# Kernel tuning notes

Measured on AMD Instinct MI355X. Metric: run time of the kernel, lower is better.

The kernel has to match this reference:

```python
import jax, jax.numpy as jnp
import numpy as np

N_HEAD = 16
D_MODEL = 1024
D_HEAD = 64
SCALE = 1.0 / D_HEAD ** 0.5
LN_EPS = 1e-5


def layer_norm(x, g, b):
    mu = jnp.mean(x, axis=-1, keepdims=True)
    var = jnp.mean(jnp.square(x - mu), axis=-1, keepdims=True)
    return (x - mu) * jax.lax.rsqrt(var + LN_EPS) * g + b


def setup_inputs() -> dict:
    key = jax.random.key(0)
    ks = jax.random.split(key, 6)
    T, B = 2048, 4
    h = jax.random.normal(ks[0], (T, B, D_MODEL), dtype=jnp.float32)
    # key-padding mask, shape (klen, bsz); True = masked
    attn_mask = jax.random.randint(ks[1], (T, B), 0, 2).astype(jnp.bool_)
    s = 1.0 / np.sqrt(D_MODEL)
    wq = jax.random.uniform(ks[2], (N_HEAD * D_HEAD, D_MODEL), minval=-s, maxval=s, dtype=jnp.float32)
    wkv = jax.random.uniform(ks[3], (2 * N_HEAD * D_HEAD, D_MODEL), minval=-s, maxval=s, dtype=jnp.float32)
    wo = jax.random.uniform(ks[4], (D_MODEL, N_HEAD * D_HEAD), minval=-s, maxval=s, dtype=jnp.float32)
    ln_g = jnp.ones((D_MODEL,), jnp.float32)
    ln_b = jnp.zeros((D_MODEL,), jnp.float32)
    return {"h": h, "attn_mask": attn_mask, "wq": wq, "wkv": wkv,
            "wo": wo, "ln_g": ln_g, "ln_b": ln_b}


def reference(h, attn_mask, wq, wkv, wo, ln_g, ln_b):
    T, B, _ = h.shape
    c = h  # mems is None
    head_q = (h @ wq.T).reshape(T, B, N_HEAD, D_HEAD)
    kv = c @ wkv.T
    head_k, head_v = jnp.split(kv, 2, axis=-1)
    head_k = head_k.reshape(T, B, N_HEAD, D_HEAD)
    head_v = head_v.reshape(T, B, N_HEAD, D_HEAD)

    # scores: [qlen, klen, bsz, n_head]
    attn_score = jnp.einsum('ibnd,jbnd->ijbn', head_q, head_k) * SCALE
    attn_score = jnp.where(attn_mask[None, :, :, None], -jnp.inf, attn_score)
    attn_prob = jax.nn.softmax(attn_score, axis=1)

    attn_vec = jnp.einsum('ijbn,jbnd->ibnd', attn_prob, head_v)
    attn_vec = attn_vec.reshape(T, B, N_HEAD * D_HEAD)
    attn_out = attn_vec @ wo.T
    # post-lnorm residual (pre_lnorm=False); gate='plus' path unused here
    return layer_norm(h + attn_out, ln_g, ln_b)
```

## Files before the change

### kernel.cpp

```cpp
#include <hip/hip_runtime.h>

#define T_LEN 2048
#define BSZ 4
#define NHEAD 16
#define DHEAD 64
#define DMODEL 1024
#define SCALE 0.125f
#define L2E_SCALE (0.125f * 1.44269504f)
#define ROW 72

typedef __bf16 bf16x8 __attribute__((ext_vector_type(8)));
typedef float f32x4 __attribute__((ext_vector_type(4)));

__device__ __forceinline__ float bf2f(unsigned short u) {
  union { unsigned int i; float f; } v; v.i = ((unsigned int)u) << 16; return v.f;
}
__device__ __forceinline__ unsigned short f2bf(float f) {
  union { float f; unsigned int i; } v; v.f = f;
  unsigned int r = v.i + 0x7fffu + ((v.i >> 16) & 1u);
  return (unsigned short)(r >> 16);
}

typedef __attribute__((address_space(1))) void* gptr_t;
typedef __attribute__((address_space(3))) void* lptr_t;

__device__ __forceinline__ void load_lds16(const void* g, void* l) {
  __builtin_amdgcn_global_load_lds((gptr_t)g, (lptr_t)l, 16, 0, 0);
}

__global__ __launch_bounds__(256) void cvt_prep(const float* __restrict__ h,
                                                const float* __restrict__ wq,
                                                const float* __restrict__ wkv,
                                                const float* __restrict__ wo,
                                                const unsigned char* __restrict__ mask,
                                                unsigned short* __restrict__ h_bf,
                                                unsigned short* __restrict__ wq_bf,
                                                unsigned short* __restrict__ wkv_bf,
                                                unsigned short* __restrict__ wo_bf,
                                                int* __restrict__ pos,
                                                int* __restrict__ nkeys) {
  const int tid = threadIdx.x;
  if (blockIdx.x < 12288) {
    const size_t E4 = (size_t)T_LEN * BSZ * DMODEL / 4;
    const size_t W4 = (size_t)NHEAD * DHEAD * DMODEL / 4;
    const size_t g = (size_t)blockIdx.x * 256 + tid;
    const float* src; unsigned short* dst; size_t off;
    if (g < E4)                { src = h;   dst = h_bf;   off = g; }
    else if (g < E4 + W4)      { src = wq;  dst = wq_bf;  off = g - E4; }
    else if (g < E4 + 3 * W4)  { src = wkv; dst = wkv_bf; off = g - E4 - W4; }
    else                       { src = wo;  dst = wo_bf;  off = g - E4 - 3 * W4; }
    const float4 v = *(const float4*)(src + off * 4);
    ushort4 o;
    o.x = f2bf(v.x); o.y = f2bf(v.y); o.z = f2bf(v.z); o.w = f2bf(v.w);
    *(ushort4*)(dst + off * 4) = o;
    return;
  }
  __shared__ int s_any;
  if (tid == 0) s_any = 0;
  __syncthreads();
  int acc = 0;
  for (int i = tid; i < T_LEN * BSZ; i += 256)
    if ((i & 3) != 0 && mask[i] != 0) acc = 1;
  if (acc) atomicOr(&s_any, 1);
  __syncthreads();
  const int mmode = s_any ? 0 : 1;
  const int wv = tid >> 6, lane = tid & 63;
  const int b = wv;
  int run = 0;
  for (int j0 = 0; j0 < T_LEN; j0 += 64) {
    const int j = j0 + lane;
    const int mval = mmode ? ((const int*)mask)[(size_t)j * BSZ + b]
                           : (int)mask[(size_t)j * BSZ + b];
    const int keep = (mval == 0) ? 1 : 0;
    int x = keep;
#pragma unroll
    for (int off = 1; off < 64; off <<= 1) {
      const int y = __shfl_up(x, off, 64);
      if (lane >= off) x += y;
    }
    pos[b * T_LEN + j] = keep ? (run + x - keep) : -1;
    run += __shfl(x, 63, 64);
  }
  if (lane == 0) nkeys[b] = run;
}

#define GEMM64_BODY(Aptr, Bptr)                                                        \
  const int tid  = threadIdx.x;                                                        \
  const int lane = tid & 63;                                                           \
  const int wv   = tid >> 6;                                                           \
  const int wr = (wv >> 1) * 64;                                                       \
  const int wc = (wv & 1) * 64;                                                        \
  const int mi   = lane & 15;                                                          \
  const int quad = lane >> 4;                                                          \
  f32x4 acc[4][4] = {};                                                                \
  int rowc[4], colc[4];                                                                \
  _Pragma("unroll")                                                                    \
  for (int c = 0; c < 4; c++) {                                                        \
    const int s = c * 256 + tid;                                                       \
    rowc[c] = s >> 3;                                                                  \
    colc[c] = ((s & 7) ^ (rowc[c] & 7)) * 8;                                           \
  }                                                                                    \
  const int swz = mi & 7;                                                              \
  for (int k0 = 0; k0 < DMODEL; k0 += 64) {                                            \
    _Pragma("unroll")                                                                  \
    for (int c = 0; c < 4; c++) {                                                      \
      load_lds16(Aptr + (size_t)rowc[c] * DMODEL + k0 + colc[c], As + c * 2048 + wv * 512); \
      load_lds16(Bptr + (size_t)rowc[c] * DMODEL + k0 + colc[c], Bs + c * 2048 + wv * 512); \
    }                                                                                  \
    __syncthreads();                                                                   \
    _Pragma("unroll")                                                                  \
    for (int kq = 0; kq < 2; kq++) {                                                   \
      const int cp = ((kq * 4 + quad) ^ swz) * 8;                                      \
      bf16x8 af[4], bfr[4];                                                            \
      _Pragma("unroll")                                                                \
      for (int rt = 0; rt < 4; rt++)                                                   \
        af[rt] = *(const bf16x8*)(As + (wr + rt * 16 + mi) * 64 + cp);                 \
      _Pragma("unroll")                                                                \
      for (int ct = 0; ct < 4; ct++)                                                   \
        bfr[ct] = *(const bf16x8*)(Bs + (wc + ct * 16 + mi) * 64 + cp);                \
      _Pragma("unroll")                                                                \
      for (int rt = 0; rt < 4; rt++)                                                   \
        _Pragma("unroll")                                                              \
        for (int ct = 0; ct < 4; ct++)                                                 \
          acc[rt][ct] = __builtin_amdgcn_mfma_f32_16x16x32_bf16(af[rt], bfr[ct], acc[rt][ct], 0, 0, 0); \
    }                                                                                  \
    __syncthreads();                                                                   \
  }

__global__ __launch_bounds__(256) void gemm_qkv(const unsigned short* __restrict__ A,
                                                const unsigned short* __restrict__ Wq,
                                                const unsigned short* __restrict__ Wkv,
                                                const int* __restrict__ pos,
                                                unsigned short* __restrict__ outQ,
                                                unsigned short* __restrict__ outK,
                                                unsigned short* __restrict__ outVt) {
  __shared__ alignas(16) unsigned short As[128 * 64];
  __shared__ alignas(16) unsigned short Bs[128 * 64];
  const int m0 = blockIdx.y * 128;
  const int n0 = blockIdx.x * 128;
  const unsigned short* Abase = A + (size_t)m0 * DMODEL;
  const unsigned short* Bbase = (n0 < DMODEL) ? (Wq + (size_t)n0 * DMODEL)
                                              : (Wkv + (size_t)(n0 - DMODEL) * DMODEL);
  GEMM64_BODY(Abase, Bbase)

  const int region = n0 >> 10;
#pragma unroll
  for (int rt = 0; rt < 4; rt++) {
#pragma unroll
    for (int r = 0; r < 4; r++) {
      const int gm = m0 + wr + rt * 16 + quad * 4 + r;
      const int i = gm >> 2, b = gm & 3;
      int p = i;
      if (region > 0) p = pos[b * T_LEN + i];
      if (region > 0 && p < 0) continue;
#pragma unroll
      for (int ct = 0; ct < 4; ct++) {
        const int gn = n0 + wc + ct * 16 + mi;
        const int gnl = gn & (DMODEL - 1);
        const int hn = gnl >> 6, d = gnl & 63;
        const float v = acc[rt][ct][r];
        if (region == 0)
          outQ[(((size_t)b * NHEAD + hn) * T_LEN + i) * DHEAD + d] = f2bf(v * L2E_SCALE);
        else if (region == 1)
          outK[(((size_t)b * NHEAD + hn) * T_LEN + p) * DHEAD + d] = f2bf(v);
        else
          outVt[(((size_t)b * NHEAD + hn) * DHEAD + d) * T_LEN + p] = f2bf(v);
      }
    }
  }
}

__global__ __launch_bounds__(256) void gemm_out(const unsigned short* __restrict__ A,
                                                const unsigned short* __restrict__ Bw,
                                                unsigned short* __restrict__ outB) {
  __shared__ alignas(16) unsigned short As[128 * 64];
  __shared__ alignas(16) unsigned short Bs[128 * 64];
  const int m0 = blockIdx.y * 128;
  const int n0 = blockIdx.x * 128;
  const unsigned short* Abase = A  + (size_t)m0 * DMODEL;
  const unsigned short* Bbase = Bw + (size_t)n0 * DMODEL;
  GEMM64_BODY(Abase, Bbase)

#pragma unroll
  for (int rt = 0; rt < 4; rt++)
#pragma unroll
    for (int ct = 0; ct < 4; ct++)
#pragma unroll
      for (int r = 0; r < 4; r++) {
        const int gm = m0 + wr + rt * 16 + quad * 4 + r;
        const int gn = n0 + wc + ct * 16 + mi;
        outB[(size_t)gm * DMODEL + gn] = f2bf(acc[rt][ct][r]);
      }
}

template<bool TAIL>
__device__ __forceinline__ void attn_chunk(int j0, int nk, int mi, int quad,
    const unsigned short* Ks, const unsigned short* Vts, unsigned short* PsW,
    const bf16x8 (&qb)[2][2], f32x4 (&oc)[2][4], float (&rs)[2]) {
  f32x4 sc[2][4] = {};
#pragma unroll
  for (int ct = 0; ct < 4; ct++) {
    const bf16x8 kf0 = *(const bf16x8*)(Ks + (ct * 16 + mi) * ROW + quad * 8);
    const bf16x8 kf1 = *(const bf16x8*)(Ks + (ct * 16 + mi) * ROW + 32 + quad * 8);
#pragma unroll
    for (int g = 0; g < 2; g++) {
      sc[g][ct] = __builtin_amdgcn_mfma_f32_16x16x32_bf16(kf0, qb[g][0], sc[g][ct], 0, 0, 0);
      sc[g][ct] = __builtin_amdgcn_mfma_f32_16x16x32_bf16(kf1, qb[g][1], sc[g][ct], 0, 0, 0);
    }
  }
#pragma unroll
  for (int g = 0; g < 2; g++)
#pragma unroll
    for (int ct = 0; ct < 4; ct++) {
#pragma unroll
      for (int r = 0; r < 4; r++) {
        float p = __builtin_amdgcn_exp2f(sc[g][ct][r]);
        if (TAIL && (j0 + ct * 16 + quad * 4 + r >= nk)) p = 0.f;
        rs[g] += p;
        sc[g][ct][r] = p;
      }
      union { float f; unsigned u; } c0, c1, c2, c3;
      c0.f = sc[g][ct][0]; c1.f = sc[g][ct][1]; c2.f = sc[g][ct][2]; c3.f = sc[g][ct][3];
      const unsigned pk0 = (c0.u >> 16) | (c1.u & 0xFFFF0000u);
      const unsigned pk1 = (c2.u >> 16) | (c3.u & 0xFFFF0000u);
      *(uint2*)(PsW + (g * 16 + mi) * ROW + ct * 16 + quad * 4) = make_uint2(pk0, pk1);
    }
  bf16x8 pa0[2], pa1[2];
#pragma unroll
  for (int g = 0; g < 2; g++) {
    pa0[g] = *(const bf16x8*)(PsW + (g * 16 + mi) * ROW + quad * 8);
    pa1[g] = *(const bf16x8*)(PsW + (g * 16 + mi) * ROW + 32 + quad * 8);
  }
#pragma unroll
  for (int ct = 0; ct < 4; ct++) {
    const bf16x8 vf0 = *(const bf16x8*)(Vts + (ct * 16 + mi) * ROW + quad * 8);
    const bf16x8 vf1 = *(const bf16x8*)(Vts + (ct * 16 + mi) * ROW + 32 + quad * 8);
#pragma unroll
    for (int g = 0; g < 2; g++) {
      oc[g][ct] = __builtin_amdgcn_mfma_f32_16x16x32_bf16(pa0[g], vf0, oc[g][ct], 0, 0, 0);
      oc[g][ct] = __builtin_amdgcn_mfma_f32_16x16x32_bf16(pa1[g], vf1, oc[g][ct], 0, 0, 0);
    }
  }
}

__global__ __launch_bounds__(256, 4) void attn_mfma(const unsigned short* __restrict__ Qg,
                                                    const unsigned short* __restrict__ Kg,
                                                    const unsigned short* __restrict__ Vtg,
                                                    const int* __restrict__ nkeys,
                                                    unsigned short* __restrict__ av) {
  __shared__ alignas(16) unsigned short smem[18688];
  unsigned short* Ks  = smem;
  unsigned short* Vts = smem + 4608;
  unsigned short* Qs  = smem + 9216;
  float* Ls = (float*)(smem + 18432);

  const int tid  = threadIdx.x;
  const int lane = tid & 63;
  const int wv   = tid >> 6;
  const int mi   = lane & 15;
  const int quad = lane >> 4;
  const int i0 = blockIdx.x * 128;
  const int b  = blockIdx.y;
  const int n  = blockIdx.z;
  const size_t base = ((size_t)b * NHEAD + n) * T_LEN * DHEAD;
  const int nk = nkeys[b];

  for (int it = tid; it < 1024; it += 256) {
    const int r = it >> 3, c8 = (it & 7) * 8;
    *(uint4*)(Qs + r * ROW + c8) = *(const uint4*)(Qg + base + (size_t)(i0 + r) * DHEAD + c8);
  }
  __syncthreads();
  bf16x8 qb[2][2];
#pragma unroll
  for (int g = 0; g < 2; g++) {
    qb[g][0] = *(const bf16x8*)(Qs + (wv * 32 + g * 16 + mi) * ROW + quad * 8);
    qb[g][1] = *(const bf16x8*)(Qs + (wv * 32 + g * 16 + mi) * ROW + 32 + quad * 8);
  }

  f32x4 oc[2][4] = {};
  float rs[2] = {0.f, 0.f};
  unsigned short* PsW = Qs + wv * 2304;

  const int nmain = nk & ~63;
  for (int j0 = 0; j0 < nmain; j0 += 64) {
    for (int it = tid; it < 512; it += 256) {
      const int r = it >> 3, c8 = (it & 7) * 8;
      *(uint4*)(Ks  + r * ROW + c8) = *(const uint4*)(Kg  + base + (size_t)(j0 + r) * DHEAD + c8);
      *(uint4*)(Vts + r * ROW + c8) = *(const uint4*)(Vtg + base + (size_t)r * T_LEN + j0 + c8);
    }
    __syncthreads();
    attn_chunk<false>(j0, nk, mi, quad, Ks, Vts, PsW, qb, oc, rs);
    __syncthreads();
  }
  if (nmain < nk) {
    for (int it = tid; it < 512; it += 256) {
      const int r = it >> 3, c8 = (it & 7) * 8;
      *(uint4*)(Ks  + r * ROW + c8) = *(const uint4*)(Kg  + base + (size_t)(nmain + r) * DHEAD + c8);
      *(uint4*)(Vts + r * ROW + c8) = *(const uint4*)(Vtg + base + (size_t)r * T_LEN + nmain + c8);
    }
    __syncthreads();
    attn_chunk<true>(nmain, nk, mi, quad, Ks, Vts, PsW, qb, oc, rs);
  }

#pragma unroll
  for (int g = 0; g < 2; g++) {
    float t = rs[g];
    t += __shfl_xor(t, 16, 64);
    t += __shfl_xor(t, 32, 64);
    rs[g] = t;
  }
  if (quad == 0) { Ls[wv * 32 + mi] = rs[0]; Ls[wv * 32 + 16 + mi] = rs[1]; }
  __syncthreads();
  float linv[2][4];
#pragma unroll
  for (int g = 0; g < 2; g++)
#pragma unroll
    for (int r = 0; r < 4; r++) {
      const float l = Ls[wv * 32 + g * 16 + quad * 4 + r];
      linv[g][r] = (l > 0.f) ? (1.f / l) : 0.f;
    }
#pragma unroll
  for (int g = 0; g < 2; g++)
#pragma unroll
    for (int ct = 0; ct < 4; ct++)
#pragma unroll
      for (int r = 0; r < 4; r++) {
        const int q = i0 + wv * 32 + g * 16 + quad * 4 + r;
        const int d = ct * 16 + mi;
        av[((size_t)q * BSZ + b) * DMODEL + n * DHEAD + d] = f2bf(oc[g][ct][r] * linv[g][r]);
      }
}

__global__ __launch_bounds__(256) void ln_kernel(const float* __restrict__ h,
                                                 const unsigned short* __restrict__ ao,
                                                 const float* __restrict__ g,
                                                 const float* __restrict__ bb,
                                                 float* __restrict__ out) {
  __shared__ float red[16];
  const int row = blockIdx.x;
  const int tid = threadIdx.x;
  const size_t base = (size_t)row * DMODEL;
  float x[4];
  float s = 0.f, sq = 0.f;
#pragma unroll
  for (int k = 0; k < 4; k++) {
    const int c = tid + k * 256;
    const float xv = h[base + c] + bf2f(ao[base + c]);
    x[k] = xv; s += xv; sq += xv * xv;
  }
#pragma unroll
  for (int off = 32; off; off >>= 1) { s += __shfl_xor(s, off, 64); sq += __shfl_xor(sq, off, 64); }
  const int wv = tid >> 6, lane = tid & 63;
  if (lane == 0) { red[wv] = s; red[8 + wv] = sq; }
  __syncthreads();
  if (tid == 0) {
    float ts = 0.f, tq = 0.f;
    for (int w = 0; w < 4; w++) { ts += red[w]; tq += red[8 + w]; }
    red[4] = ts; red[12] = tq;
  }
  __syncthreads();
  const float mu  = red[4] * (1.f / DMODEL);
  const float var = red[12] * (1.f / DMODEL) - mu * mu;
  const float inv = rsqrtf(var + 1e-5f);
#pragma unroll
  for (int k = 0; k < 4; k++) {
    const int c = tid + k * 256;
    out[base + c] = (x[k] - mu) * inv * g[c] + bb[c];
  }
}

extern "C" void kernel_launch(void* const* d_in, const int* in_sizes, int n_in,
                              void* d_out, int out_size, void* d_ws, size_t ws_size,
                              hipStream_t stream) {
  (void)in_sizes; (void)n_in; (void)out_size; (void)ws_size;
  const float* h           = (const float*)d_in[0];
  const unsigned char* msk = (const unsigned char*)d_in[1];
  const float* wq          = (const float*)d_in[2];
  const float* wkv         = (const float*)d_in[3];
  const float* wo          = (const float*)d_in[4];
  const float* lng         = (const float*)d_in[5];
  const float* lnb         = (const float*)d_in[6];
  float* out = (float*)d_out;

  const size_t E  = (size_t)T_LEN * BSZ * DMODEL;
  const size_t WQ = (size_t)NHEAD * DHEAD * DMODEL;
  char* ws = (char*)d_ws;
  int* nkeys            = (int*)ws;                       ws += 16;
  int* pos              = (int*)ws;                       ws += (size_t)BSZ * T_LEN * 4;
  unsigned short* h_bf  = (unsigned short*)ws;            ws += E * 2;
  unsigned short* wq_bf = (unsigned short*)ws;            ws += WQ * 2;
  unsigned short* wkv_bf= (unsigned short*)ws;            ws += 2 * WQ * 2;
  unsigned short* wo_bf = (unsigned short*)ws;            ws += WQ * 2;
  unsigned short* Qb    = (unsigned short*)ws;            ws += E * 2;
  unsigned short* Kb    = (unsigned short*)ws;            ws += E * 2;
  unsigned short* Vtb   = (unsigned short*)ws;            ws += E * 2;
  unsigned short* AV    = (unsigned short*)ws;            ws += E * 2;
  unsigned short* AO    = (unsigned short*)ws;

  const dim3 blk(256);
  cvt_prep<<<dim3(12289), blk, 0, stream>>>(h, wq, wkv, wo, msk,
                                            h_bf, wq_bf, wkv_bf, wo_bf, pos, nkeys);
  gemm_qkv<<<dim3(3 * DMODEL / 128, T_LEN * BSZ / 128), blk, 0, stream>>>(
      h_bf, wq_bf, wkv_bf, pos, Qb, Kb, Vtb);
  attn_mfma<<<dim3(T_LEN / 128, BSZ, NHEAD), blk, 0, stream>>>(Qb, Kb, Vtb, nkeys, AV);
  gemm_out<<<dim3(DMODEL / 128, T_LEN * BSZ / 128), blk, 0, stream>>>(AV, wo_bf, AO);
  ln_kernel<<<dim3(T_LEN * BSZ), blk, 0, stream>>>(h, AO, lng, lnb, out);
}
```

Baseline: 319.9 us.

## Double-buffer LDS tiles in GEMMs and vectorize layernorm loads/stores

The shared GEMM body now uses two LDS buffers, issuing global-to-LDS loads for the next K-tile before computing on the current one. This hides load latency and needs one barrier per iteration instead of two. The price is twice the LDS per block (64KB), which may lower occupancy. Separately, the layernorm kernel now uses float4 and ushort4 vector loads and stores instead of strided scalar accesses.

```diff
diff --git a/kernel.cpp b/kernel.cpp
--- a/kernel.cpp
+++ b/kernel.cpp
@@ -84,7 +84,7 @@
   if (lane == 0) nkeys[b] = run;
 }
 
-#define GEMM64_BODY(Aptr, Bptr)                                                        \
+#define GEMM64_DBUF(Aptr, Bptr)                                                        \
   const int tid  = threadIdx.x;                                                        \
   const int lane = tid & 63;                                                           \
   const int wv   = tid >> 6;                                                           \
@@ -101,30 +101,41 @@
     colc[c] = ((s & 7) ^ (rowc[c] & 7)) * 8;                                           \
   }                                                                                    \
   const int swz = mi & 7;                                                              \
+  _Pragma("unroll")                                                                    \
+  for (int c = 0; c < 4; c++) {                                                        \
+    load_lds16(Aptr + (size_t)rowc[c] * DMODEL + colc[c], As + c * 2048 + wv * 512);   \
+    load_lds16(Bptr + (size_t)rowc[c] * DMODEL + colc[c], Bs + c * 2048 + wv * 512);   \
+  }                                                                                    \
   for (int k0 = 0; k0 < DMODEL; k0 += 64) {                                            \
-    _Pragma("unroll")                                                                  \
-    for (int c = 0; c < 4; c++) {                                                      \
-      load_lds16(Aptr + (size_t)rowc[c] * DMODEL + k0 + colc[c], As + c * 2048 + wv * 512); \
-      load_lds16(Bptr + (size_t)rowc[c] * DMODEL + k0 + colc[c], Bs + c * 2048 + wv * 512); \
+    const int cur = (k0 >> 6) & 1;                                                     \
+    const unsigned short* Asr = As + cur * 8192;                                       \
+    const unsigned short* Bsr = Bs + cur * 8192;                                       \
+    unsigned short* Asw = As + (1 - cur) * 8192;                                       \
+    unsigned short* Bsw = Bs + (1 - cur) * 8192;                                       \
+    __syncthreads();                                                                   \
+    if (k0 + 64 < DMODEL) {                                                            \
+      _Pragma("unroll")                                                                \
+      for (int c = 0; c < 4; c++) {                                                    \
+        load_lds16(Aptr + (size_t)rowc[c] * DMODEL + k0 + 64 + colc[c], Asw + c * 2048 + wv * 512); \
+        load_lds16(Bptr + (size_t)rowc[c] * DMODEL + k0 + 64 + colc[c], Bsw + c * 2048 + wv * 512); \
+      }                                                                                \
     }                                                                                  \
-    __syncthreads();                                                                   \
     _Pragma("unroll")                                                                  \
     for (int kq = 0; kq < 2; kq++) {                                                   \
       const int cp = ((kq * 4 + quad) ^ swz) * 8;                                      \
       bf16x8 af[4], bfr[4];                                                            \
       _Pragma("unroll")                                                                \
       for (int rt = 0; rt < 4; rt++)                                                   \
-        af[rt] = *(const bf16x8*)(As + (wr + rt * 16 + mi) * 64 + cp);                 \
+        af[rt] = *(const bf16x8*)(Asr + (wr + rt * 16 + mi) * 64 + cp);                \
       _Pragma("unroll")                                                                \
       for (int ct = 0; ct < 4; ct++)                                                   \
-        bfr[ct] = *(const bf16x8*)(Bs + (wc + ct * 16 + mi) * 64 + cp);                \
+        bfr[ct] = *(const bf16x8*)(Bsr + (wc + ct * 16 + mi) * 64 + cp);               \
       _Pragma("unroll")                                                                \
       for (int rt = 0; rt < 4; rt++)                                                   \
         _Pragma("unroll")                                                              \
         for (int ct = 0; ct < 4; ct++)                                                 \
           acc[rt][ct] = __builtin_amdgcn_mfma_f32_16x16x32_bf16(af[rt], bfr[ct], acc[rt][ct], 0, 0, 0); \
     }                                                                                  \
-    __syncthreads();                                                                   \
   }
 
 __global__ __launch_bounds__(256) void gemm_qkv(const unsigned short* __restrict__ A,
@@ -134,14 +145,14 @@
                                                 unsigned short* __restrict__ outQ,
                                                 unsigned short* __restrict__ outK,
                                                 unsigned short* __restrict__ outVt) {
-  __shared__ alignas(16) unsigned short As[128 * 64];
-  __shared__ alignas(16) unsigned short Bs[128 * 64];
+  __shared__ alignas(16) unsigned short As[2 * 128 * 64];
+  __shared__ alignas(16) unsigned short Bs[2 * 128 * 64];
   const int m0 = blockIdx.y * 128;
   const int n0 = blockIdx.x * 128;
   const unsigned short* Abase = A + (size_t)m0 * DMODEL;
   const unsigned short* Bbase = (n0 < DMODEL) ? (Wq + (size_t)n0 * DMODEL)
                                               : (Wkv + (size_t)(n0 - DMODEL) * DMODEL);
-  GEMM64_BODY(Abase, Bbase)
+  GEMM64_DBUF(Abase, Bbase)
 
   const int region = n0 >> 10;
 #pragma unroll
@@ -173,13 +184,13 @@
 __global__ __launch_bounds__(256) void gemm_out(const unsigned short* __restrict__ A,
                                                 const unsigned short* __restrict__ Bw,
                                                 unsigned short* __restrict__ outB) {
-  __shared__ alignas(16) unsigned short As[128 * 64];
-  __shared__ alignas(16) unsigned short Bs[128 * 64];
+  __shared__ alignas(16) unsigned short As[2 * 128 * 64];
+  __shared__ alignas(16) unsigned short Bs[2 * 128 * 64];
   const int m0 = blockIdx.y * 128;
   const int n0 = blockIdx.x * 128;
   const unsigned short* Abase = A  + (size_t)m0 * DMODEL;
   const unsigned short* Bbase = Bw + (size_t)n0 * DMODEL;
-  GEMM64_BODY(Abase, Bbase)
+  GEMM64_DBUF(Abase, Bbase)
 
 #pragma unroll
   for (int rt = 0; rt < 4; rt++)
@@ -340,14 +351,13 @@
   const int row = blockIdx.x;
   const int tid = threadIdx.x;
   const size_t base = (size_t)row * DMODEL;
-  float x[4];
+  const int c = tid * 4;
+  const float4 hv = *(const float4*)(h + base + c);
+  const ushort4 a4 = *(const ushort4*)(ao + base + c);
+  float x[4] = { hv.x + bf2f(a4.x), hv.y + bf2f(a4.y), hv.z + bf2f(a4.z), hv.w + bf2f(a4.w) };
   float s = 0.f, sq = 0.f;
 #pragma unroll
-  for (int k = 0; k < 4; k++) {
-    const int c = tid + k * 256;
-    const float xv = h[base + c] + bf2f(ao[base + c]);
-    x[k] = xv; s += xv; sq += xv * xv;
-  }
+  for (int k = 0; k < 4; k++) { s += x[k]; sq += x[k] * x[k]; }
 #pragma unroll
   for (int off = 32; off; off >>= 1) { s += __shfl_xor(s, off, 64); sq += __shfl_xor(sq, off, 64); }
   const int wv = tid >> 6, lane = tid & 63;
@@ -362,11 +372,14 @@
   const float mu  = red[4] * (1.f / DMODEL);
   const float var = red[12] * (1.f / DMODEL) - mu * mu;
   const float inv = rsqrtf(var + 1e-5f);
-#pragma unroll
-  for (int k = 0; k < 4; k++) {
-    const int c = tid + k * 256;
-    out[base + c] = (x[k] - mu) * inv * g[c] + bb[c];
-  }
+  const float4 gv = *(const float4*)(g + c);
+  const float4 bv = *(const float4*)(bb + c);
+  float4 o;
+  o.x = (x[0] - mu) * inv * gv.x + bv.x;
+  o.y = (x[1] - mu) * inv * gv.y + bv.y;
+  o.z = (x[2] - mu) * inv * gv.z + bv.z;
+  o.w = (x[3] - mu) * inv * gv.w + bv.w;
+  *(float4*)(out + base + c) = o;
 }
 
 extern "C" void kernel_launch(void* const* d_in, const int* in_sizes, int n_in,
```

Measured after the change: 313.2 us. -2.1%, faster.
